# Performance work log

Measured on AMD Instinct MI355X. Metric: run time of the kernel, lower is better.

The kernel has to match this reference:

```python
import jax, jax.numpy as jnp
import numpy as np

B, L, DIN, W, H, NL = 4, 1024, 768, 12288, 8, 2
BOTTLENECK = 64
DB = W // BOTTLENECK        # 192: total bottlenecked attention dim
HD = DB // H                # 24: per-head dim
K = 32                      # topk
LAM = 1.0 / (4 * DIN)
EPS = 1e-6


def setup_inputs() -> dict:
    key = jax.random.key(0)
    ks = jax.random.split(key, 8)
    x_input = jax.random.normal(ks[0], (B, L, DIN), jnp.float32)
    # decoder dictionary (torch: randn; scaled for numeric stability)
    D = jax.random.normal(ks[1], (W, DIN), jnp.float32) * 0.02
    b = jnp.zeros((1, DIN), jnp.float32)
    # per-attn-layer bottlenecked projections, stacked over layers
    Wq = jax.random.normal(ks[2], (NL, W, DB), jnp.float32) * 0.02
    Wk = jax.random.normal(ks[3], (NL, W, DB), jnp.float32) * 0.02
    Wv = jax.random.normal(ks[4], (NL, W, DB), jnp.float32) * 0.02
    Wo = jax.random.normal(ks[5], (NL, DB, W), jnp.float32) * 0.02
    bq = jnp.zeros((NL, DB), jnp.float32)
    bk = jnp.zeros((NL, DB), jnp.float32)
    bv = jnp.zeros((NL, DB), jnp.float32)
    bo = jnp.zeros((NL, W), jnp.float32)
    return {"x_input": x_input, "D": D, "b": b, "Wq": Wq, "bq": bq,
            "Wk": Wk, "bk": bk, "Wv": Wv, "bv": bv, "Wo": Wo, "bo": bo}


def _attention(z_ctx, z_in, Wq, bq, Wk, bk, Wv, bv, Wo, bo):
    # queries from current codes, keys/values from shifted context codes
    q = (z_in @ Wq + bq).reshape(B, L, H, HD)
    k = (z_ctx @ Wk + bk).reshape(B, L, H, HD)
    v = (z_ctx @ Wv + bv).reshape(B, L, H, HD)
    scores = jnp.einsum('bqhd,bkhd->bhqk', q, k) / np.sqrt(HD).astype(np.float32)
    causal = jnp.tril(jnp.ones((L, L), bool))  # query t sees ctx positions <= t
    scores = jnp.where(causal, scores, jnp.float32(-1e30))
    a = jax.nn.softmax(scores, axis=-1)
    o = jnp.einsum('bhqk,bkhd->bqhd', a, v).reshape(B, L, DB)
    return o @ Wo + bo


def reference(x_input, D, b, Wq, bq, Wk, bk, Wv, bv, Wo, bo):
    E = D.T  # tied weights
    x = x_input - b
    z_pred = jnp.zeros((B, L, W), x.dtype)
    for i in range(NL):
        z_in = jax.nn.relu((x * LAM) @ E)                       # [B,L,W]
        z_ctx = jnp.concatenate([jnp.zeros_like(z_in[:, :1]), z_in[:, :-1]], axis=1)
        z_pred_ = jax.nn.relu(_attention(z_ctx, z_in, Wq[i], bq[i], Wk[i], bk[i],
                                         Wv[i], bv[i], Wo[i], bo[i]))
        Dz = z_pred_ @ D                                        # [B,L,DIN]
        Dz_norm = jnp.linalg.norm(Dz, axis=-1, keepdims=True) + EPS
        proj_scale = jnp.sum(Dz * x, axis=-1, keepdims=True) / (Dz_norm ** 2)
        z_pred = z_pred + z_pred_ * proj_scale
        x = x - proj_scale * Dz
    # topk sparsification of the novel codes
    z_novel = jax.nn.relu((x * LAM) @ E)
    zf = z_novel.reshape(-1, W)                                 # [B*L, W]
    _, idx = jax.lax.top_k(zf, K)
    mask = jnp.zeros_like(zf).at[jnp.arange(zf.shape[0])[:, None], idx].set(1.0)
    z_novel = (zf * mask).reshape(B, L, W)
    x_recons = (z_novel + z_pred) @ D + b
    return x_recons
```

## Files before the change

### kernel.cpp

```cpp
#include <hip/hip_runtime.h>
#include <hip/hip_bf16.h>

typedef __attribute__((ext_vector_type(4))) float f32x4;
typedef __attribute__((ext_vector_type(8))) short short8;
typedef __attribute__((ext_vector_type(8))) unsigned short ushort8;
typedef __attribute__((ext_vector_type(4))) unsigned short ushort4v;
typedef __attribute__((ext_vector_type(4))) unsigned int uint4v;

#define DEVFN __device__ __forceinline__

DEVFN float b2f(unsigned short u) { return __uint_as_float(((unsigned)u) << 16); }
DEVFN unsigned short f2b(float f) {
  __hip_bfloat16 h = __float2bfloat16(f);
  return __builtin_bit_cast(unsigned short, h);
}

DEVFN void load_lds16(const void* g, void* l) {
  __builtin_amdgcn_global_load_lds(
      (const __attribute__((address_space(1))) unsigned int*)g,
      (__attribute__((address_space(3))) unsigned int*)l, 16, 0, 0);
}


__global__ void fill_out_zero(float* o, int n) {
  int i = blockIdx.x * 256 + threadIdx.x;
  if (i < n) o[i] = 0.0f;
}

__global__ __launch_bounds__(256) void init_x(
    const float* __restrict__ xin, const float* __restrict__ bvec,
    float* __restrict__ x, unsigned short* __restrict__ xb) {
  size_t i = (size_t)blockIdx.x * 256 + threadIdx.x;
  int col = (int)(i % 768);
  float v = xin[i] - bvec[col];
  x[i] = v;
  xb[i] = f2b(v);
}

__global__ __launch_bounds__(256) void fill_bias(
    float* __restrict__ buf, const float* __restrict__ bias, int ld) {
  size_t i = (size_t)blockIdx.x * 256 + threadIdx.x;
  buf[i] = bias ? bias[(int)(i % ld)] : 0.0f;
}

__global__ __launch_bounds__(256) void conv_f2b(
    const float* __restrict__ in, unsigned short* __restrict__ out) {
  size_t i = ((size_t)blockIdx.x * 256 + threadIdx.x) * 4;
  f32x4 v = *(const f32x4*)(in + i);
  ushort4v w;
#pragma unroll
  for (int e = 0; e < 4; ++e) w[e] = f2b(v[e]);
  *(ushort4v*)(out + i) = w;
}

__global__ __launch_bounds__(256) void transpose_f2b(
    const float* __restrict__ in, unsigned short* __restrict__ out,
    int R, int C) {
  __shared__ float tile[32][33];
  int r0 = blockIdx.x * 32, c0 = blockIdx.y * 32;
  int tx = threadIdx.x & 31, ty = threadIdx.x >> 5;
#pragma unroll
  for (int i = 0; i < 4; ++i)
    tile[ty + i * 8][tx] = in[(size_t)(r0 + ty + i * 8) * C + c0 + tx];
  __syncthreads();
#pragma unroll
  for (int i = 0; i < 4; ++i)
    out[(size_t)(c0 + ty + i * 8) * R + r0 + tx] = f2b(tile[tx][ty + i * 8]);
}

template <int GX, int GY, int GZ, int RX, int RG>
DEVFN void rect_decode(int bid, int& x, int& y, int& z) {
  constexpr int NRG = (GY * GZ) / RG;
  const int xcd = bid & 7;
  const int rr = bid >> 3;
  const int rgx = xcd % NRG, rxx = xcd / NRG;
  const int gl = rr % RG, xl = rr / RG;
  const int g = rgx * RG + gl;
  x = rxx * RX + xl;
  y = g % GY;
  z = g / GY;
}

template <typename CT, bool RELU, int SC, bool BIAS, bool SPLITK,
          int GX, int GY, int GZ, int RX, int RG>
__global__ __launch_bounds__(256) void gemm_bt2(
    const unsigned short* __restrict__ A, const unsigned short* __restrict__ B,
    CT* __restrict__ C, const float* __restrict__ bias,
    int K, int ldc, float alpha) {
  __shared__ unsigned short sA[2][128 * 64];
  __shared__ unsigned short sB[2][128 * 64];
  const int tid = threadIdx.x;
  const int wave = tid >> 6, lane = tid & 63;
  int bx, by, bz;
  rect_decode<GX, GY, GZ, RX, RG>((int)blockIdx.x, bx, by, bz);
  const int row0 = bx * 128, col0 = by * 128;
  const unsigned short* Ab = A + (size_t)row0 * K;
  const unsigned short* Bb = B + (size_t)col0 * K;
  const int srow = lane >> 3;
  const int swc = ((lane & 7) ^ srow) * 8;
  const int wm = wave & 1, wn = wave >> 1;
  const int lr = lane & 15;
  const int hi = lane >> 4;
  const int l7 = lane & 7;
  const int ksw0 = (hi ^ l7) * 8;
  const int ksw1 = ((4 + hi) ^ l7) * 8;
  const int klen = SPLITK ? (K / GZ) : K;
  const int kbeg = SPLITK ? bz * klen : 0;
  const int nt = klen / 64;
  f32x4 acc[4][4] = {};
  auto stage = [&](int buf, int t) {
    const int k0 = kbeg + t * 64;
#pragma unroll
    for (int it = 0; it < 4; ++it) {
      int chunk = wave * 4 + it;
      int r = chunk * 8 + srow;
      load_lds16(Ab + (size_t)r * K + k0 + swc, &sA[buf][chunk * 512]);
      load_lds16(Bb + (size_t)r * K + k0 + swc, &sB[buf][chunk * 512]);
    }
  };
  stage(0, 0);
  __syncthreads();
  for (int t = 0; t < nt; ++t) {
    const int cur = t & 1;
    if (t + 1 < nt) stage(cur ^ 1, t + 1);
    const unsigned short* cA = &sA[cur][0];
    const unsigned short* cB = &sB[cur][0];
#pragma unroll
    for (int ks = 0; ks < 2; ++ks) {
      const int ko = ks ? ksw1 : ksw0;
      short8 af[4], bfr[4];
#pragma unroll
      for (int i = 0; i < 4; ++i)
        af[i] = *(const short8*)&cA[(wm * 64 + i * 16 + lr) * 64 + ko];
#pragma unroll
      for (int i = 0; i < 4; ++i)
        bfr[i] = *(const short8*)&cB[(wn * 64 + i * 16 + lr) * 64 + ko];
#pragma unroll
      for (int i = 0; i < 4; ++i)
#pragma unroll
        for (int j = 0; j < 4; ++j)
          acc[i][j] = __builtin_amdgcn_mfma_f32_16x16x32_bf16(af[i], bfr[j], acc[i][j], 0, 0, 0);
    }
    __syncthreads();
  }
  const int rc = (SC == 0) ? 0 : ((row0 >> 10) + 1);
  const int rbase = row0 + rc + wm * 64 + (lane >> 4) * 4;
  const int cbase = col0 + wn * 64 + lr;
#pragma unroll
  for (int j = 0; j < 4; ++j) {
    int col = cbase + j * 16;
    float bv = BIAS ? bias[col] : 0.0f;
#pragma unroll
    for (int i = 0; i < 4; ++i) {
#pragma unroll
      for (int r = 0; r < 4; ++r) {
        float vv = acc[i][j][r] * alpha;
        size_t off = (size_t)(rbase + i * 16 + r) * ldc + col;
        if constexpr (SPLITK) {
          atomicAdd((float*)C + off, vv);
        } else {
          vv += bv;
          if (RELU) vv = fmaxf(vv, 0.0f);
          if constexpr (sizeof(CT) == 2) ((unsigned short*)C)[off] = f2b(vv);
          else C[off] = vv;
        }
      }
    }
  }
}

__global__ __launch_bounds__(256) void gemm_qkv(
    const unsigned short* __restrict__ A, const unsigned short* __restrict__ Bq,
    float* __restrict__ qb, float* __restrict__ kb, float* __restrict__ vb) {
  __shared__ unsigned short sA[2][128 * 64];
  __shared__ unsigned short sB[2][192 * 64];
  const int tid = threadIdx.x;
  const int wave = tid >> 6, lane = tid & 63;
  const int bid = (int)blockIdx.x;
  const int xcd = bid & 7;
  const int rr = bid >> 3;
  const int rgx = xcd % 2, rxx = xcd / 2;
  const int gl = rr % 12, xl = rr / 12;
  const int g = rgx * 12 + gl;
  const int bx = rxx * 8 + xl;
  const int wz = g % 3;
  const int ky = g / 3;
  const int shift = (wz > 0);
  const unsigned short* B = Bq + (size_t)wz * 192 * 12288;
  float* C = (wz == 0) ? qb : (wz == 1 ? kb : vb);
  const int row0 = bx * 128;
  const int ra = (row0 >> 10) + 1;
  const unsigned short* Ab = A + (size_t)(row0 + ra) * 12288;
  const int srow = lane >> 3;
  const int swc = ((lane & 7) ^ srow) * 8;
  const int wm = wave & 1, wn = wave >> 1;
  const int lr = lane & 15;
  const int hi = lane >> 4;
  const int l7 = lane & 7;
  const int ksw0 = (hi ^ l7) * 8;
  const int ksw1 = ((4 + hi) ^ l7) * 8;
  const int kbeg = ky * 1536;
  f32x4 acc[4][6] = {};
  auto stage = [&](int buf, int t) {
    const int k0 = kbeg + t * 64;
#pragma unroll
    for (int it = 0; it < 10; ++it) {
      int c = wave * 10 + it;
      if (c < 16) {
        int r = c * 8 + srow;
        load_lds16(Ab + (size_t)r * 12288 + k0 + swc, &sA[buf][c * 512]);
      } else {
        int cb = c - 16;
        int r = cb * 8 + srow;
        load_lds16(B + (size_t)r * 12288 + k0 + swc, &sB[buf][cb * 512]);
      }
    }
  };
  stage(0, 0);
  __syncthreads();
  for (int t = 0; t < 24; ++t) {
    const int cur = t & 1;
    if (t + 1 < 24) stage(cur ^ 1, t + 1);
    const unsigned short* cA = &sA[cur][0];
    const unsigned short* cB = &sB[cur][0];
#pragma unroll
    for (int ks = 0; ks < 2; ++ks) {
      const int ko = ks ? ksw1 : ksw0;
      short8 af[4], bfr[6];
#pragma unroll
      for (int i = 0; i < 4; ++i)
        af[i] = *(const short8*)&cA[(wm * 64 + i * 16 + lr) * 64 + ko];
#pragma unroll
      for (int j = 0; j < 6; ++j)
        bfr[j] = *(const short8*)&cB[(wn * 96 + j * 16 + lr) * 64 + ko];
#pragma unroll
      for (int i = 0; i < 4; ++i)
#pragma unroll
        for (int j = 0; j < 6; ++j)
          acc[i][j] = __builtin_amdgcn_mfma_f32_16x16x32_bf16(af[i], bfr[j], acc[i][j], 0, 0, 0);
    }
    __syncthreads();
  }
  const int rbase = row0 + wm * 64 + (lane >> 4) * 4;
  const int cbase = wn * 96 + lr;
#pragma unroll
  for (int j = 0; j < 6; ++j) {
    int col = cbase + j * 16;
#pragma unroll
    for (int i = 0; i < 4; ++i)
#pragma unroll
      for (int r = 0; r < 4; ++r) {
        int rw = rbase + i * 16 + r;
        if (shift) {
          if ((rw & 1023) == 1023) continue;
          rw += 1;
        }
        atomicAdd(C + (size_t)rw * 192 + col, acc[i][j][r]);
      }
  }
}

__global__ __launch_bounds__(256) void attn_pass1(
    const float* __restrict__ q, const float* __restrict__ k,
    const float* __restrict__ v, float* __restrict__ P) {
  const int wave = threadIdx.x >> 6, lane = threadIdx.x & 63;
  const int task = (int)blockIdx.x * 4 + wave;
  const int bh = task / 288, t = task % 288;
  const int b = bh >> 3, h = bh & 7;
  int g8 = 0;
  while (4 * (g8 + 1) * (g8 + 2) <= t) ++g8;
  const int r = t - 4 * g8 * (g8 + 1);
  const int qg = g8 * 8 + r / (g8 + 1);
  const int chunk = r % (g8 + 1);
  const int qi = lane & 15, ks = lane >> 4;
  const int qpos = qg * 16 + qi;
  const int n = b * 1024 + qpos;
  const float scale = 0.20412414523193154f;
  float qv[24];
  const float* qr = q + (size_t)n * 192 + h * 24;
#pragma unroll
  for (int d = 0; d < 24; ++d) qv[d] = qr[d] * scale;
  float m = -1e30f, l = 0.0f, ov[24] = {};
  const float* kbp = k + (size_t)b * 1024 * 192 + h * 24;
  const float* vbp = v + (size_t)b * 1024 * 192 + h * 24;
  const int kend = min(qpos, chunk * 128 + 127);
  for (int kp = chunk * 128 + ks; kp <= kend; kp += 4) {
    const f32x4* kr = (const f32x4*)(kbp + (size_t)kp * 192);
    float s0 = 0.0f, s1 = 0.0f, s2 = 0.0f;
#pragma unroll
    for (int j = 0; j < 2; ++j) {
      f32x4 k0 = kr[j * 3 + 0], k1 = kr[j * 3 + 1], k2 = kr[j * 3 + 2];
#pragma unroll
      for (int e = 0; e < 4; ++e) {
        s0 += qv[(j * 3 + 0) * 4 + e] * k0[e];
        s1 += qv[(j * 3 + 1) * 4 + e] * k1[e];
        s2 += qv[(j * 3 + 2) * 4 + e] * k2[e];
      }
    }
    float s = s0 + s1 + s2;
    float mn = fmaxf(m, s);
    float corr = __expf(m - mn);
    float p = __expf(s - mn);
    const f32x4* vr = (const f32x4*)(vbp + (size_t)kp * 192);
    l = l * corr + p;
#pragma unroll
    for (int j = 0; j < 6; ++j) {
      f32x4 vvv = vr[j];
#pragma unroll
      for (int e = 0; e < 4; ++e) ov[j * 4 + e] = ov[j * 4 + e] * corr + p * vvv[e];
    }
    m = mn;
  }
#pragma unroll
  for (int off = 16; off < 64; off <<= 1) {
    float m2 = __shfl_xor(m, off);
    float l2 = __shfl_xor(l, off);
    float mn = fmaxf(m, m2);
    float c1 = __expf(m - mn), c2 = __expf(m2 - mn);
    l = l * c1 + l2 * c2;
#pragma unroll
    for (int d = 0; d < 24; ++d) {
      float o2 = __shfl_xor(ov[d], off);
      ov[d] = ov[d] * c1 + o2 * c2;
    }
    m = mn;
  }
  if (ks == 0) {
    float* pr = P + ((size_t)task * 16 + qi) * 28;
    pr[0] = m;
    pr[1] = l;
#pragma unroll
    for (int d = 0; d < 24; ++d) pr[2 + d] = ov[d];
  }
}

__global__ __launch_bounds__(192) void attn_merge(
    const float* __restrict__ P, unsigned short* __restrict__ o) {
  const int n = blockIdx.x;
  const int tid = threadIdx.x;
  const int h = tid / 24, d = tid - h * 24;
  const int b = n >> 10, qpos = n & 1023;
  const int qg = qpos >> 4, qi = qpos & 15;
  const int g8 = qg >> 3;
  const int nch = g8 + 1;
  const int bh = b * 8 + h;
  const int base = bh * 288 + 4 * g8 * (g8 + 1) + (qg - g8 * 8) * (g8 + 1);
  float M = -1e30f;
  for (int c = 0; c < nch; ++c)
    M = fmaxf(M, P[((size_t)(base + c) * 16 + qi) * 28]);
  float L = 0.0f, OV = 0.0f;
  for (int c = 0; c < nch; ++c) {
    const float* pr = P + ((size_t)(base + c) * 16 + qi) * 28;
    float w = __expf(pr[0] - M);
    L += pr[1] * w;
    OV += pr[2 + d] * w;
  }
  o[(size_t)n * 192 + h * 24 + d] = f2b(OV / L);
}

__global__ __launch_bounds__(256) void proj_update(
    const float* __restrict__ Dz, float* __restrict__ x,
    unsigned short* __restrict__ xb) {
  const int n = blockIdx.x;
  const int tid = threadIdx.x;
  const float* dz = Dz + (size_t)n * 768;
  float* xr = x + (size_t)n * 768;
  float dot = 0.0f, s2 = 0.0f;
  for (int i = tid; i < 768; i += 256) {
    float a = dz[i], c = xr[i];
    dot += a * c;
    s2 += a * a;
  }
#pragma unroll
  for (int o2 = 32; o2; o2 >>= 1) {
    dot += __shfl_down(dot, o2);
    s2 += __shfl_down(s2, o2);
  }
  __shared__ float sd[4], ss[4], sp;
  const int wave = tid >> 6, lane = tid & 63;
  if (lane == 0) { sd[wave] = dot; ss[wave] = s2; }
  __syncthreads();
  if (tid == 0) {
    float Dd = sd[0] + sd[1] + sd[2] + sd[3];
    float S = ss[0] + ss[1] + ss[2] + ss[3];
    float nrm = sqrtf(S) + 1e-6f;
    sp = Dd / (nrm * nrm);
  }
  __syncthreads();
  float p = sp;
  for (int i = tid; i < 768; i += 256) {
    float nx = xr[i] - p * dz[i];
    xr[i] = nx;
    xb[(size_t)n * 768 + i] = f2b(nx);
  }
}

DEVFN int sanitize(int v) { return (v & 0x8000) ? 0 : v; }

__global__ __launch_bounds__(256) void topk_rows(
    const unsigned short* __restrict__ zbuf, int* __restrict__ idxo,
    float* __restrict__ valo) {
  const int n = blockIdx.x;
  const int b = n >> 10;
  const int tid = threadIdx.x;
  const int wave = tid >> 6, lane = tid & 63;
  const uint4v* zr = (const uint4v*)(zbuf + (size_t)(n + b + 1) * 12288);
  uint4v pk[6];
#pragma unroll
  for (int j = 0; j < 6; ++j) pk[j] = zr[tid * 6 + j];
  __shared__ int swsum[4];
  __shared__ int seq[256];
  __shared__ int spcnt;
  int lo = 0, hi = 0x7F7F;
  while (lo < hi) {
    int mid = (lo + hi) >> 1;
    int c = 0;
#pragma unroll
    for (int j = 0; j < 6; ++j)
#pragma unroll
      for (int e = 0; e < 4; ++e) {
        unsigned int u = pk[j][e];
        c += (sanitize((int)(u & 0xffffu)) > mid) + (sanitize((int)(u >> 16)) > mid);
      }
#pragma unroll
    for (int o2 = 32; o2; o2 >>= 1) c += __shfl_down(c, o2);
    if (lane == 0) swsum[wave] = c;
    __syncthreads();
    int total = swsum[0] + swsum[1] + swsum[2] + swsum[3];
    __syncthreads();
    if (total < 32) hi = mid; else lo = mid + 1;
  }
  const int T = lo;
  int cgt = 0, ceq = 0;
#pragma unroll
  for (int j = 0; j < 6; ++j)
#pragma unroll
    for (int e = 0; e < 4; ++e) {
      unsigned int u = pk[j][e];
      int v0 = sanitize((int)(u & 0xffffu)), v1 = sanitize((int)(u >> 16));
      cgt += (v0 > T) + (v1 > T);
      ceq += (v0 == T) + (v1 == T);
    }
  int cg = cgt;
#pragma unroll
  for (int o2 = 32; o2; o2 >>= 1) cg += __shfl_down(cg, o2);
  if (lane == 0) swsum[wave] = cg;
  seq[tid] = ceq;
  if (tid == 0) spcnt = 0;
  __syncthreads();
  const int total_gt = swsum[0] + swsum[1] + swsum[2] + swsum[3];
  for (int o2 = 1; o2 < 256; o2 <<= 1) {
    int vv = (tid >= o2) ? seq[tid - o2] : 0;
    __syncthreads();
    seq[tid] += vv;
    __syncthreads();
  }
  const int quota = 32 - total_gt;
  int rank = seq[tid] - ceq;
  int* irow = idxo + (size_t)n * 32;
  float* vrow = valo + (size_t)n * 32;
#pragma unroll
  for (int j = 0; j < 6; ++j)
#pragma unroll
    for (int e = 0; e < 4; ++e) {
      unsigned int u = pk[j][e];
#pragma unroll
      for (int hf = 0; hf < 2; ++hf) {
        int v = sanitize(hf ? (int)(u >> 16) : (int)(u & 0xffffu));
        bool kp = false;
        if (v > T) kp = true;
        else if (v == T) { if (rank < quota) kp = true; ++rank; }
        if (kp) {
          int pos = atomicAdd(&spcnt, 1);
          irow[pos] = tid * 48 + j * 8 + e * 2 + hf;
          vrow[pos] = b2f((unsigned short)v);
        }
      }
    }
}

__global__ __launch_bounds__(256) void sparse_recons(
    const int* __restrict__ idxo, const float* __restrict__ valo,
    const float* __restrict__ x, const float* __restrict__ xin,
    const float* __restrict__ D, float* __restrict__ out) {
  const int n = blockIdx.x;
  const int t = threadIdx.x;
  __shared__ int sidx[32];
  __shared__ float sval[32];
  if (t < 32) { sidx[t] = idxo[(size_t)n * 32 + t]; sval[t] = valo[(size_t)n * 32 + t]; }
  __syncthreads();
  float acc[3];
#pragma unroll
  for (int u = 0; u < 3; ++u) {
    size_t i = (size_t)n * 768 + t + u * 256;
    acc[u] = xin[i] - x[i];
  }
  for (int j = 0; j < 32; ++j) {
    size_t base = (size_t)sidx[j] * 768;
    float vj = sval[j];
#pragma unroll
    for (int u = 0; u < 3; ++u) acc[u] += vj * D[base + t + u * 256];
  }
#pragma unroll
  for (int u = 0; u < 3; ++u) out[(size_t)n * 768 + t + u * 256] = acc[u];
}

extern "C" void kernel_launch(void* const* d_in, const int* in_sizes, int n_in,
                              void* d_out, int out_size, void* d_ws, size_t ws_size,
                              hipStream_t stream) {
  (void)in_sizes; (void)n_in;
  const float* xin  = (const float*)d_in[0];
  const float* D    = (const float*)d_in[1];
  const float* bvec = (const float*)d_in[2];
  const float* Wq   = (const float*)d_in[3];
  const float* bq   = (const float*)d_in[4];
  const float* Wk   = (const float*)d_in[5];
  const float* bk   = (const float*)d_in[6];
  const float* Wv   = (const float*)d_in[7];
  const float* bv   = (const float*)d_in[8];
  const float* Wo   = (const float*)d_in[9];
  const float* bo   = (const float*)d_in[10];
  const float LAM = 1.0f / 3072.0f;

  char* ws = (char*)d_ws;
  size_t off = 0;
  auto alloc = [&](size_t bytes) {
    void* p = ws + off;
    off += (bytes + 255) & ~(size_t)255;
    return p;
  };
  unsigned short* zbuf = (unsigned short*)alloc((size_t)4 * 1025 * 12288 * 2);
  unsigned short* zpred_ = zbuf;
  float* attnP = (float*)zbuf;
  float* x           = (float*)alloc((size_t)4096 * 768 * 4);
  unsigned short* xb = (unsigned short*)alloc((size_t)4096 * 768 * 2);
  float* qb  = (float*)alloc((size_t)4096 * 192 * 4);
  float* kb  = (float*)alloc((size_t)4096 * 192 * 4);
  float* vb  = (float*)alloc((size_t)4096 * 192 * 4);
  unsigned short* ob = (unsigned short*)alloc((size_t)4096 * 192 * 2);
  float* Dz  = (float*)alloc((size_t)4096 * 768 * 4);
  int* idxo  = (int*)alloc((size_t)4096 * 32 * 4);
  float* valo = (float*)alloc((size_t)4096 * 32 * 4);
  const size_t WQKV = (size_t)192 * 12288;
  unsigned short* WqkvT = (unsigned short*)alloc((size_t)6 * WQKV * 2);
  unsigned short* WoT   = (unsigned short*)alloc((size_t)2 * 12288 * 192 * 2);
  unsigned short* Dbt   = (unsigned short*)alloc((size_t)12288 * 768 * 2);
  unsigned short* Dt    = (unsigned short*)alloc((size_t)768 * 12288 * 2);
  const size_t NEED = off;

  if (ws_size < NEED) {
    fill_out_zero<<<(out_size + 255) / 256, 256, 0, stream>>>((float*)d_out, out_size);
    return;
  }

  init_x<<<12288, 256, 0, stream>>>(xin, bvec, x, xb);
  conv_f2b<<<9216, 256, 0, stream>>>(D, Dbt);
  transpose_f2b<<<dim3(384, 24), 256, 0, stream>>>(D, Dt, 12288, 768);
  for (int l = 0; l < 2; ++l) {
    transpose_f2b<<<dim3(384, 6), 256, 0, stream>>>(
        Wq + (size_t)l * 12288 * 192, WqkvT + (size_t)(l * 3 + 0) * WQKV, 12288, 192);
    transpose_f2b<<<dim3(384, 6), 256, 0, stream>>>(
        Wk + (size_t)l * 12288 * 192, WqkvT + (size_t)(l * 3 + 1) * WQKV, 12288, 192);
    transpose_f2b<<<dim3(384, 6), 256, 0, stream>>>(
        Wv + (size_t)l * 12288 * 192, WqkvT + (size_t)(l * 3 + 2) * WQKV, 12288, 192);
    transpose_f2b<<<dim3(6, 384), 256, 0, stream>>>(
        Wo + (size_t)l * 192 * 12288, WoT + (size_t)l * 12288 * 192, 192, 12288);
  }

  for (int l = 0; l < 2; ++l) {
    gemm_bt2<unsigned short, true, 1, false, false, 32, 96, 1, 16, 24>
        <<<3072, 256, 0, stream>>>(xb, Dbt, zbuf, nullptr, 768, 12288, LAM);
    fill_bias<<<3072, 256, 0, stream>>>(qb, bq + (size_t)l * 192, 192);
    fill_bias<<<3072, 256, 0, stream>>>(kb, bk + (size_t)l * 192, 192);
    fill_bias<<<3072, 256, 0, stream>>>(vb, bv + (size_t)l * 192, 192);
    gemm_qkv<<<768, 256, 0, stream>>>(
        zbuf, WqkvT + (size_t)(l * 3) * WQKV, qb, kb, vb);
    attn_pass1<<<2304, 256, 0, stream>>>(qb, kb, vb, attnP);
    attn_merge<<<4096, 192, 0, stream>>>(attnP, ob);
    gemm_bt2<unsigned short, true, 0, true, false, 32, 96, 1, 16, 24>
        <<<3072, 256, 0, stream>>>(
        ob, WoT + (size_t)l * 12288 * 192, zpred_, bo + (size_t)l * 12288, 192, 12288, 1.0f);
    fill_bias<<<12288, 256, 0, stream>>>(Dz, nullptr, 768);
    gemm_bt2<float, false, 0, false, true, 32, 6, 4, 16, 6>
        <<<768, 256, 0, stream>>>(zpred_, Dt, Dz, nullptr, 12288, 768, 1.0f);
    proj_update<<<4096, 256, 0, stream>>>(Dz, x, xb);
  }
  gemm_bt2<unsigned short, true, 1, false, false, 32, 96, 1, 16, 24>
      <<<3072, 256, 0, stream>>>(xb, Dbt, zbuf, nullptr, 768, 12288, LAM);
  topk_rows<<<4096, 256, 0, stream>>>(zbuf, idxo, valo);
  sparse_recons<<<4096, 256, 0, stream>>>(idxo, valo, x, xin, D, (float*)d_out);
}
```

Measured before the change: 1.479 ms.

## Restructure QKV GEMM to two-way split-K with plain stores and merge

The QKV projection GEMM now uses 64-row tiles and splits K into two halves instead of eight, writing partial results with plain stores: the first half goes to the q/k/v buffers with bias added, the second to a scratch buffer. A separate merge kernel adds the two. This removes the float atomicAdd traffic and the q bias fill, at the cost of an extra scratch write and read and a longer per-block K loop. The tile-order decode in gemm_bt2 also staggers the x index per XCD group, which changes cache locality across blocks.

```diff
diff --git a/kernel.cpp b/kernel.cpp
--- a/kernel.cpp
+++ b/kernel.cpp
@@ -74,7 +74,9 @@
   const int xcd = bid & 7;
   const int rr = bid >> 3;
   const int rgx = xcd % NRG, rxx = xcd / NRG;
-  const int gl = rr % RG, xl = rr / RG;
+  const int gl = rr % RG;
+  int xl = rr / RG;
+  xl = (xl + rgx * (RX / NRG)) % RX;
   const int g = rgx * RG + gl;
   x = rxx * RX + xl;
   y = g % GY;
@@ -171,24 +173,28 @@
 
 __global__ __launch_bounds__(256) void gemm_qkv(
     const unsigned short* __restrict__ A, const unsigned short* __restrict__ Bq,
-    float* __restrict__ qb, float* __restrict__ kb, float* __restrict__ vb) {
-  __shared__ unsigned short sA[2][128 * 64];
+    const float* __restrict__ bq, const float* __restrict__ bk,
+    const float* __restrict__ bv,
+    float* __restrict__ qb, float* __restrict__ kb, float* __restrict__ vb,
+    float* __restrict__ P2) {
+  __shared__ unsigned short sA[2][64 * 64];
   __shared__ unsigned short sB[2][192 * 64];
   const int tid = threadIdx.x;
   const int wave = tid >> 6, lane = tid & 63;
   const int bid = (int)blockIdx.x;
   const int xcd = bid & 7;
   const int rr = bid >> 3;
-  const int rgx = xcd % 2, rxx = xcd / 2;
-  const int gl = rr % 12, xl = rr / 12;
-  const int g = rgx * 12 + gl;
-  const int bx = rxx * 8 + xl;
-  const int wz = g % 3;
-  const int ky = g / 3;
+  const int grank = xcd * 48 + rr;
+  const int combo = grank >> 6;
+  const int row = grank & 63;
+  const int wz = combo >> 1;
+  const int s = combo & 1;
   const int shift = (wz > 0);
   const unsigned short* B = Bq + (size_t)wz * 192 * 12288;
-  float* C = (wz == 0) ? qb : (wz == 1 ? kb : vb);
-  const int row0 = bx * 128;
+  const float* bias = (wz == 0) ? bq : (wz == 1 ? bk : bv);
+  float* dst = (s == 0) ? ((wz == 0) ? qb : (wz == 1 ? kb : vb))
+                        : (P2 + (size_t)wz * 786432);
+  const int row0 = row * 64;
   const int ra = (row0 >> 10) + 1;
   const unsigned short* Ab = A + (size_t)(row0 + ra) * 12288;
   const int srow = lane >> 3;
@@ -199,18 +205,18 @@
   const int l7 = lane & 7;
   const int ksw0 = (hi ^ l7) * 8;
   const int ksw1 = ((4 + hi) ^ l7) * 8;
-  const int kbeg = ky * 1536;
-  f32x4 acc[4][6] = {};
+  const int kbeg = s * 6144;
+  f32x4 acc[2][6] = {};
   auto stage = [&](int buf, int t) {
     const int k0 = kbeg + t * 64;
 #pragma unroll
-    for (int it = 0; it < 10; ++it) {
-      int c = wave * 10 + it;
-      if (c < 16) {
+    for (int it = 0; it < 8; ++it) {
+      int c = wave * 8 + it;
+      if (c < 8) {
         int r = c * 8 + srow;
         load_lds16(Ab + (size_t)r * 12288 + k0 + swc, &sA[buf][c * 512]);
       } else {
-        int cb = c - 16;
+        int cb = c - 8;
         int r = cb * 8 + srow;
         load_lds16(B + (size_t)r * 12288 + k0 + swc, &sB[buf][cb * 512]);
       }
@@ -218,36 +224,37 @@
   };
   stage(0, 0);
   __syncthreads();
-  for (int t = 0; t < 24; ++t) {
+  for (int t = 0; t < 96; ++t) {
     const int cur = t & 1;
-    if (t + 1 < 24) stage(cur ^ 1, t + 1);
+    if (t + 1 < 96) stage(cur ^ 1, t + 1);
     const unsigned short* cA = &sA[cur][0];
     const unsigned short* cB = &sB[cur][0];
 #pragma unroll
     for (int ks = 0; ks < 2; ++ks) {
       const int ko = ks ? ksw1 : ksw0;
-      short8 af[4], bfr[6];
-#pragma unroll
-      for (int i = 0; i < 4; ++i)
-        af[i] = *(const short8*)&cA[(wm * 64 + i * 16 + lr) * 64 + ko];
+      short8 af[2], bfr[6];
+#pragma unroll
+      for (int i = 0; i < 2; ++i)
+        af[i] = *(const short8*)&cA[(wm * 32 + i * 16 + lr) * 64 + ko];
 #pragma unroll
       for (int j = 0; j < 6; ++j)
         bfr[j] = *(const short8*)&cB[(wn * 96 + j * 16 + lr) * 64 + ko];
 #pragma unroll
-      for (int i = 0; i < 4; ++i)
+      for (int i = 0; i < 2; ++i)
 #pragma unroll
         for (int j = 0; j < 6; ++j)
           acc[i][j] = __builtin_amdgcn_mfma_f32_16x16x32_bf16(af[i], bfr[j], acc[i][j], 0, 0, 0);
     }
     __syncthreads();
   }
-  const int rbase = row0 + wm * 64 + (lane >> 4) * 4;
+  const int rbase = row0 + wm * 32 + (lane >> 4) * 4;
   const int cbase = wn * 96 + lr;
 #pragma unroll
   for (int j = 0; j < 6; ++j) {
     int col = cbase + j * 16;
-#pragma unroll
-    for (int i = 0; i < 4; ++i)
+    float bvv = (s == 0) ? bias[col] : 0.0f;
+#pragma unroll
+    for (int i = 0; i < 2; ++i)
 #pragma unroll
       for (int r = 0; r < 4; ++r) {
         int rw = rbase + i * 16 + r;
@@ -255,9 +262,23 @@
           if ((rw & 1023) == 1023) continue;
           rw += 1;
         }
-        atomicAdd(C + (size_t)rw * 192 + col, acc[i][j][r]);
+        dst[(size_t)rw * 192 + col] = acc[i][j][r] + bvv;
       }
   }
+}
+
+__global__ __launch_bounds__(256) void qkv_merge(
+    const float* __restrict__ P2, float* __restrict__ qb,
+    float* __restrict__ kb, float* __restrict__ vb) {
+  size_t i = ((size_t)blockIdx.x * 256 + threadIdx.x) * 4;
+  const int plane = (int)(i / 786432);
+  const size_t o = i - (size_t)plane * 786432;
+  float* dst = plane == 0 ? qb : (plane == 1 ? kb : vb);
+  f32x4 a = *(const f32x4*)(P2 + i);
+  f32x4 b = *(const f32x4*)(dst + o);
+#pragma unroll
+  for (int e = 0; e < 4; ++e) b[e] += a[e];
+  *(f32x4*)(dst + o) = b;
 }
 
 __global__ __launch_bounds__(256) void attn_pass1(
@@ -547,6 +568,7 @@
   unsigned short* Dbt   = (unsigned short*)alloc((size_t)12288 * 768 * 2);
   unsigned short* Dt    = (unsigned short*)alloc((size_t)768 * 12288 * 2);
   const size_t NEED = off;
+  float* P2 = Dz;
 
   if (ws_size < NEED) {
     fill_out_zero<<<(out_size + 255) / 256, 256, 0, stream>>>((float*)d_out, out_size);
@@ -570,11 +592,14 @@
   for (int l = 0; l < 2; ++l) {
     gemm_bt2<unsigned short, true, 1, false, false, 32, 96, 1, 16, 24>
         <<<3072, 256, 0, stream>>>(xb, Dbt, zbuf, nullptr, 768, 12288, LAM);
-    fill_bias<<<3072, 256, 0, stream>>>(qb, bq + (size_t)l * 192, 192);
     fill_bias<<<3072, 256, 0, stream>>>(kb, bk + (size_t)l * 192, 192);
     fill_bias<<<3072, 256, 0, stream>>>(vb, bv + (size_t)l * 192, 192);
-    gemm_qkv<<<768, 256, 0, stream>>>(
-        zbuf, WqkvT + (size_t)(l * 3) * WQKV, qb, kb, vb);
+    fill_bias<<<9216, 256, 0, stream>>>(P2, nullptr, 192);
+    gemm_qkv<<<384, 256, 0, stream>>>(
+        zbuf, WqkvT + (size_t)(l * 3) * WQKV,
+        bq + (size_t)l * 192, bk + (size_t)l * 192, bv + (size_t)l * 192,
+        qb, kb, vb, P2);
+    qkv_merge<<<2304, 256, 0, stream>>>(P2, qb, kb, vb);
     attn_pass1<<<2304, 256, 0, stream>>>(qb, kb, vb, attnP);
     attn_merge<<<4096, 192, 0, stream>>>(attnP, ob);
     gemm_bt2<unsigned short, true, 0, true, false, 32, 96, 1, 16, 24>
```

After: 1.417 ms. 1.04x faster.
